# Optimization experiments

Hardware: AMD Instinct MI355X
Metric: run time of the kernel (lower is better)

## Reference

```python
import jax, jax.numpy as jnp
import numpy as np

D_MODEL = 2048
N_HEADS = 16
N_KV = 4
HEAD_DIM = D_MODEL // N_HEADS  # 128
KV_DIM = N_KV * HEAD_DIM       # 512
CLIP = 8.0
EPS = 1e-5
THETA = 500000.0


def setup_inputs() -> dict:
    key = jax.random.key(0)
    ks = jax.random.split(key, 12)
    B, T = 2, 2048
    std = 0.02
    return {
        "x": jax.random.normal(ks[0], (B, T, D_MODEL), jnp.float32),
        "wq": jax.random.normal(ks[1], (D_MODEL, D_MODEL), jnp.float32) * std,
        "bq": jnp.zeros((D_MODEL,), jnp.float32),
        "wk": jax.random.normal(ks[2], (KV_DIM, D_MODEL), jnp.float32) * std,
        "bk": jnp.zeros((KV_DIM,), jnp.float32),
        "wv": jax.random.normal(ks[3], (KV_DIM, D_MODEL), jnp.float32) * std,
        "bv": jnp.zeros((KV_DIM,), jnp.float32),
        "wo": jax.random.normal(ks[4], (D_MODEL, D_MODEL), jnp.float32) * std,
        "bo": jnp.zeros((D_MODEL,), jnp.float32),
        "q_gamma": jnp.ones((D_MODEL,), jnp.float32),
        "q_beta": jnp.zeros((D_MODEL,), jnp.float32),
        "k_gamma": jnp.ones((KV_DIM,), jnp.float32),
        "k_beta": jnp.zeros((KV_DIM,), jnp.float32),
    }


def _layernorm(x, gamma, beta):
    mu = jnp.mean(x, axis=-1, keepdims=True)
    var = jnp.mean(jnp.square(x - mu), axis=-1, keepdims=True)
    return (x - mu) * jax.lax.rsqrt(var + EPS) * gamma + beta


def _rope(q, k):
    # q: (B,T,H,Dh), k: (B,T,Hkv,Dh); non-interleaved rotate-half RoPE
    T = q.shape[1]
    half = HEAD_DIM // 2
    inv_freq = 1.0 / (THETA ** (jnp.arange(0, half, dtype=jnp.float32) * 2.0 / HEAD_DIM))
    freqs = jnp.arange(T, dtype=jnp.float32)[:, None] * inv_freq[None, :]  # (T, half)
    emb = jnp.concatenate([freqs, freqs], axis=-1)  # (T, Dh)
    cos = jnp.cos(emb)[None, :, None, :]
    sin = jnp.sin(emb)[None, :, None, :]

    def rot_half(x):
        x1, x2 = x[..., :half], x[..., half:]
        return jnp.concatenate([-x2, x1], axis=-1)

    q = q * cos + rot_half(q) * sin
    k = k * cos + rot_half(k) * sin
    return q, k


def reference(x, wq, bq, wk, bk, wv, bv, wo, bo, q_gamma, q_beta, k_gamma, k_beta):
    B, T, _ = x.shape
    q = x @ wq.T + bq            # (B,T,D)
    k = x @ wk.T + bk            # (B,T,KV_DIM)
    v = x @ wv.T + bv
    q = jnp.clip(q, -CLIP, CLIP)
    k = jnp.clip(k, -CLIP, CLIP)
    v = jnp.clip(v, -CLIP, CLIP)
    q = _layernorm(q, q_gamma, q_beta)
    k = _layernorm(k, k_gamma, k_beta)
    q = q.reshape(B, T, N_HEADS, HEAD_DIM)
    k = k.reshape(B, T, N_KV, HEAD_DIM)
    v = v.reshape(B, T, N_KV, HEAD_DIM)
    q, k = _rope(q, k)
    # to (B,H,T,Dh)
    q = q.transpose(0, 2, 1, 3)
    k = k.transpose(0, 2, 1, 3)
    v = v.transpose(0, 2, 1, 3)
    g = N_HEADS // N_KV
    # GQA repeat_interleave via broadcast: (B,Hkv,T,Dh) -> (B,H,T,Dh)
    k = jnp.broadcast_to(k[:, :, None], (B, N_KV, g, T, HEAD_DIM)).reshape(B, N_HEADS, T, HEAD_DIM)
    v = jnp.broadcast_to(v[:, :, None], (B, N_KV, g, T, HEAD_DIM)).reshape(B, N_HEADS, T, HEAD_DIM)
    scale = 1.0 / jnp.sqrt(jnp.float32(HEAD_DIM))
    scores = jnp.einsum('bhqd,bhkd->bhqk', q, k) * scale
    causal = jnp.tril(jnp.ones((T, T), dtype=bool))
    scores = jnp.where(causal[None, None], scores, jnp.finfo(scores.dtype).min)
    att = jax.nn.softmax(scores, axis=-1)
    out = jnp.einsum('bhqk,bhkd->bhqd', att, v)     # (B,H,T,Dh)
    out = out.transpose(0, 2, 1, 3).reshape(B, T, D_MODEL)
    return out @ wo.T + bo
```

## Files before the change

### kernel.cpp

```cpp
#include <hip/hip_runtime.h>
#include <hip/hip_bf16.h>
#include <math.h>

typedef __bf16 bf16;
typedef __attribute__((ext_vector_type(8))) bf16 bf16x8;
typedef __attribute__((ext_vector_type(2))) bf16 bf16x2;
typedef __attribute__((ext_vector_type(4))) float f32x4;

#define LOG2E 1.4426950408889634f
#define LOG2_THETA 18.931568569324174f

#if __has_builtin(__builtin_amdgcn_exp2f)
#define EXP2F __builtin_amdgcn_exp2f
#else
#define EXP2F exp2f
#endif

__device__ inline void async_cp16(const void* gptr, void* lptr) {
  __builtin_amdgcn_global_load_lds(
      (const __attribute__((address_space(1))) unsigned int*)gptr,
      (__attribute__((address_space(3))) unsigned int*)lptr, 16, 0, 0);
}

__global__ __launch_bounds__(256) void cast_f32_bf16(
    const float* __restrict__ in, bf16* __restrict__ out, int n) {
  const int i = (blockIdx.x * 256 + threadIdx.x) * 8;
  if (i >= n) return;
  float4 a = *(const float4*)(in + i);
  float4 b = *(const float4*)(in + i + 4);
  bf16x8 o;
  o[0] = (bf16)a.x; o[1] = (bf16)a.y; o[2] = (bf16)a.z; o[3] = (bf16)a.w;
  o[4] = (bf16)b.x; o[5] = (bf16)b.y; o[6] = (bf16)b.z; o[7] = (bf16)b.w;
  *(bf16x8*)(out + i) = o;
}

__global__ __launch_bounds__(256) void gemm_qkv(
    const bf16* __restrict__ A, const bf16* __restrict__ W,
    const float* __restrict__ bq, const float* __restrict__ bk,
    const float* __restrict__ bv, bf16* __restrict__ C,
    int M, int N, int K) {
  __shared__ bf16 As[128 * 32];
  __shared__ bf16 Bs[128 * 32];
  const int m0 = blockIdx.x * 128, n0 = blockIdx.y * 128;
  const int t = threadIdx.x;
  const int w = t >> 6, lane = t & 63, quad = lane >> 4, l15 = lane & 15;
  const int wm = (w >> 1) * 64, wn = (w & 1) * 64;

  f32x4 acc[4][4];
#pragma unroll
  for (int i = 0; i < 4; i++)
#pragma unroll
    for (int j = 0; j < 4; j++) acc[i][j] = (f32x4)0.0f;

  const int rS = t >> 2;
  const int cS = (t & 3) * 8;

  for (int k0 = 0; k0 < K; k0 += 32) {
    async_cp16(A + (size_t)(m0 + rS) * K + k0 + cS, (char*)As + (size_t)(w * 64) * 16);
    async_cp16(A + (size_t)(m0 + 64 + rS) * K + k0 + cS, (char*)As + (size_t)(256 + w * 64) * 16);
    async_cp16(W + (size_t)(n0 + rS) * K + k0 + cS, (char*)Bs + (size_t)(w * 64) * 16);
    async_cp16(W + (size_t)(n0 + 64 + rS) * K + k0 + cS, (char*)Bs + (size_t)(256 + w * 64) * 16);
    __syncthreads();

    bf16x8 af[4], bfr[4];
#pragma unroll
    for (int i = 0; i < 4; i++)
      af[i] = *(const bf16x8*)(As + (wm + i * 16 + l15) * 32 + quad * 8);
#pragma unroll
    for (int j = 0; j < 4; j++)
      bfr[j] = *(const bf16x8*)(Bs + (wn + j * 16 + l15) * 32 + quad * 8);
#pragma unroll
    for (int i = 0; i < 4; i++)
#pragma unroll
      for (int j = 0; j < 4; j++)
        acc[i][j] = __builtin_amdgcn_mfma_f32_16x16x32_bf16(af[i], bfr[j], acc[i][j], 0, 0, 0);
    __syncthreads();
  }

#pragma unroll
  for (int i = 0; i < 4; i++)
#pragma unroll
    for (int j = 0; j < 4; j++) {
      const int col = n0 + wn + j * 16 + l15;
      float bval;
      if (col < 2048) bval = bq[col];
      else if (col < 2560) bval = bk[col - 2048];
      else bval = bv[col - 2560];
#pragma unroll
      for (int r = 0; r < 4; r++) {
        const int row = m0 + wm + i * 16 + quad * 4 + r;
        float v = acc[i][j][r] + bval;
        v = fminf(fmaxf(v, -8.0f), 8.0f);
        C[(size_t)row * N + col] = (bf16)v;
      }
    }
}

template <typename OUT_T, bool CLIP>
__global__ __launch_bounds__(256) void gemm_bt(
    const bf16* __restrict__ A, const bf16* __restrict__ W,
    const float* __restrict__ bias, OUT_T* __restrict__ C,
    int M, int N, int K) {
  __shared__ bf16 As[128 * 32];
  __shared__ bf16 Bs[128 * 32];
  const int m0 = blockIdx.x * 128, n0 = blockIdx.y * 128;
  const int t = threadIdx.x;
  const int w = t >> 6, lane = t & 63, quad = lane >> 4, l15 = lane & 15;
  const int wm = (w >> 1) * 64, wn = (w & 1) * 64;

  f32x4 acc[4][4];
#pragma unroll
  for (int i = 0; i < 4; i++)
#pragma unroll
    for (int j = 0; j < 4; j++) acc[i][j] = (f32x4)0.0f;

  const int rS = t >> 2;
  const int cS = (t & 3) * 8;

  for (int k0 = 0; k0 < K; k0 += 32) {
    async_cp16(A + (size_t)(m0 + rS) * K + k0 + cS, (char*)As + (size_t)(w * 64) * 16);
    async_cp16(A + (size_t)(m0 + 64 + rS) * K + k0 + cS, (char*)As + (size_t)(256 + w * 64) * 16);
    async_cp16(W + (size_t)(n0 + rS) * K + k0 + cS, (char*)Bs + (size_t)(w * 64) * 16);
    async_cp16(W + (size_t)(n0 + 64 + rS) * K + k0 + cS, (char*)Bs + (size_t)(256 + w * 64) * 16);
    __syncthreads();

    bf16x8 af[4], bfr[4];
#pragma unroll
    for (int i = 0; i < 4; i++)
      af[i] = *(const bf16x8*)(As + (wm + i * 16 + l15) * 32 + quad * 8);
#pragma unroll
    for (int j = 0; j < 4; j++)
      bfr[j] = *(const bf16x8*)(Bs + (wn + j * 16 + l15) * 32 + quad * 8);
#pragma unroll
    for (int i = 0; i < 4; i++)
#pragma unroll
      for (int j = 0; j < 4; j++)
        acc[i][j] = __builtin_amdgcn_mfma_f32_16x16x32_bf16(af[i], bfr[j], acc[i][j], 0, 0, 0);
    __syncthreads();
  }

#pragma unroll
  for (int i = 0; i < 4; i++)
#pragma unroll
    for (int j = 0; j < 4; j++) {
      const int col = n0 + wn + j * 16 + l15;
      const float bval = bias[col];
#pragma unroll
      for (int r = 0; r < 4; r++) {
        const int row = m0 + wm + i * 16 + quad * 4 + r;
        float v = acc[i][j][r] + bval;
        if (CLIP) v = fminf(fmaxf(v, -8.0f), 8.0f);
        C[(size_t)row * N + col] = (OUT_T)v;
      }
    }
}

__global__ __launch_bounds__(256) void ln_rope_q(
    const bf16* __restrict__ X, const float* __restrict__ gamma,
    const float* __restrict__ beta, bf16* __restrict__ Q) {
  const int row = blockIdx.x;
  const int b = row >> 11, tpos = row & 2047;
  const bf16* x = X + (size_t)row * 3072;
  __shared__ float sh[2048];
  __shared__ float red[8];
  const int tid = threadIdx.x;
  const int w = tid >> 6, lane = tid & 63;

  bf16x8 xi = *(const bf16x8*)(x + tid * 8);
  float v[8];
  float s = 0.0f;
#pragma unroll
  for (int e = 0; e < 8; e++) { v[e] = (float)xi[e]; s += v[e]; }
#pragma unroll
  for (int m = 32; m >= 1; m >>= 1) s += __shfl_xor(s, m, 64);
  if (lane == 0) red[w] = s;
  __syncthreads();
  const float mean = (red[0] + red[1] + red[2] + red[3]) * (1.0f / 2048.0f);
  float vs = 0.0f;
#pragma unroll
  for (int e = 0; e < 8; e++) { float d = v[e] - mean; vs += d * d; }
#pragma unroll
  for (int m = 32; m >= 1; m >>= 1) vs += __shfl_xor(vs, m, 64);
  if (lane == 0) red[4 + w] = vs;
  __syncthreads();
  const float var = (red[4] + red[5] + red[6] + red[7]) * (1.0f / 2048.0f);
  const float rstd = rsqrtf(var + 1e-5f);
#pragma unroll
  for (int e = 0; e < 8; e++) {
    const int c = tid * 8 + e;
    const float y = (v[e] - mean) * rstd * gamma[c] + beta[c];
    sh[c] = y; v[e] = y;
  }
  __syncthreads();

  const int c0 = tid * 8;
  const int h = c0 >> 7;
  bf16x8 ov;
#pragma unroll
  for (int e = 0; e < 8; e++) {
    const int c = c0 + e, d = c & 127, i = d & 63;
    const float inv = exp2f((float)i * (-LOG2_THETA / 64.0f));
    float sn, cs;
    sincosf((float)tpos * inv, &sn, &cs);
    const float rot = (d < 64) ? -sh[c + 64] : sh[c - 64];
    ov[e] = (bf16)(v[e] * cs + rot * sn);
  }
  *(bf16x8*)(Q + ((size_t)(b * 16 + h) * 2048 + tpos) * 128 + (c0 & 127)) = ov;
}

__global__ __launch_bounds__(256) void ln_rope_k(
    const bf16* __restrict__ X, const float* __restrict__ gamma,
    const float* __restrict__ beta, bf16* __restrict__ Ko) {
  const int row = blockIdx.x;
  const int b = row >> 11, tpos = row & 2047;
  const bf16* x = X + (size_t)row * 3072 + 2048;
  __shared__ float sh[512];
  __shared__ float red[8];
  const int tid = threadIdx.x;
  const int w = tid >> 6, lane = tid & 63;

  bf16x2 xi = *(const bf16x2*)(x + tid * 2);
  float v0 = (float)xi[0], v1 = (float)xi[1];
  float s = v0 + v1;
#pragma unroll
  for (int m = 32; m >= 1; m >>= 1) s += __shfl_xor(s, m, 64);
  if (lane == 0) red[w] = s;
  __syncthreads();
  const float mean = (red[0] + red[1] + red[2] + red[3]) * (1.0f / 512.0f);
  float d0 = v0 - mean, d1 = v1 - mean;
  float vs = d0 * d0 + d1 * d1;
#pragma unroll
  for (int m = 32; m >= 1; m >>= 1) vs += __shfl_xor(vs, m, 64);
  if (lane == 0) red[4 + w] = vs;
  __syncthreads();
  const float var = (red[4] + red[5] + red[6] + red[7]) * (1.0f / 512.0f);
  const float rstd = rsqrtf(var + 1e-5f);
  const int c0 = tid * 2;
  float y0 = d0 * rstd * gamma[c0] + beta[c0];
  float y1 = d1 * rstd * gamma[c0 + 1] + beta[c0 + 1];
  sh[c0] = y0; sh[c0 + 1] = y1;
  __syncthreads();

  const int kv = c0 >> 7;
  float yy[2] = {y0, y1};
  bf16x2 ov;
#pragma unroll
  for (int e = 0; e < 2; e++) {
    const int c = c0 + e, d = c & 127, i = d & 63;
    const float inv = exp2f((float)i * (-LOG2_THETA / 64.0f));
    float sn, cs;
    sincosf((float)tpos * inv, &sn, &cs);
    const float rot = (d < 64) ? -sh[c + 64] : sh[c - 64];
    ov[e] = (bf16)(yy[e] * cs + rot * sn);
  }
  *(bf16x2*)(Ko + ((size_t)(b * 4 + kv) * 2048 + tpos) * 128 + (c0 & 127)) = ov;
}

__global__ __launch_bounds__(256) void transpose_v(
    const bf16* __restrict__ V, bf16* __restrict__ Vt) {
  const int t0 = blockIdx.x * 64, kv = blockIdx.y, b = blockIdx.z;
  __shared__ bf16 tile[64][136];
  const int tid = threadIdx.x;
#pragma unroll
  for (int i = 0; i < 4; i++) {
    const int c = i * 256 + tid;
    const int r = c >> 4, d8 = (c & 15) * 8;
    *(bf16x8*)&tile[r][d8] =
        *(const bf16x8*)(V + (size_t)(b * 2048 + t0 + r) * 3072 + 2560 + kv * 128 + d8);
  }
  __syncthreads();
#pragma unroll
  for (int i = 0; i < 4; i++) {
    const int c = i * 256 + tid;
    const int d = c >> 3, t8 = (c & 7) * 8;
    bf16x8 o;
#pragma unroll
    for (int j = 0; j < 8; j++) o[j] = tile[t8 + j][d];
    *(bf16x8*)(Vt + (size_t)((b * 4 + kv) * 128 + d) * 2048 + t0 + t8) = o;
  }
}

__global__ __launch_bounds__(256) void flash_attn(
    const bf16* __restrict__ Q, const bf16* __restrict__ Kt,
    const bf16* __restrict__ Vt, bf16* __restrict__ O) {
  const int p = blockIdx.x;
  const int h = blockIdx.y, b = blockIdx.z;
  const int kv = h >> 2;
  const int tid = threadIdx.x;
  const int w = tid >> 6, lane = tid & 63, quad = lane >> 4, l15 = lane & 15;

  __shared__ bf16 Ks[64][128];
  __shared__ bf16 Vs[128][64];
  __shared__ bf16 Ps[4][16][88];

  const bf16* Kb = Kt + (size_t)(b * 4 + kv) * 2048 * 128;
  const bf16* Vb = Vt + (size_t)(b * 4 + kv) * 128 * 2048;

  const int ksl = lane & 15, krt = lane >> 4;
  const int vsl = lane & 7,  vdt = lane >> 3;
  int okff[4], ovff[4];
#pragma unroll
  for (int i = 0; i < 4; i++) {
    const int c = w * 4 + i;
    const int rt = c * 4 + krt;
    okff[i] = rt * 128 + ((ksl ^ (rt & 15)) * 8);
    const int d = c * 8 + vdt;
    ovff[i] = d * 2048 + ((vsl ^ (d & 7)) * 8);
  }

  const float cexp = 0.08838834764831845f * LOG2E;
  bf16x8 ones;
#pragma unroll
  for (int i = 0; i < 8; i++) ones[i] = (bf16)1.0f;

#pragma unroll 1
  for (int pass = 0; pass < 2; pass++) {
    const int qb = (pass == 0) ? (31 - p) : p;
    const int q0 = qb * 64;
    const int nkt = qb + 1;

    const bf16* Qb = Q + ((size_t)(b * 16 + h) * 2048 + q0 + w * 16 + l15) * 128;
    bf16x8 aq[4];
#pragma unroll
    for (int kk = 0; kk < 4; kk++) aq[kk] = *(const bf16x8*)(Qb + kk * 32 + quad * 8);

    f32x4 o[9];
#pragma unroll
    for (int dt = 0; dt < 9; dt++) o[dt] = (f32x4)0.0f;

#pragma unroll 1
    for (int kt = 0; kt < nkt; kt++) {
      const int k0 = kt * 64;
      __syncthreads();
      {
        const size_t kbase = (size_t)k0 * 128;
#pragma unroll
        for (int i = 0; i < 4; i++) {
          const int c = w * 4 + i;
          async_cp16(Kb + kbase + okff[i], (char*)&Ks[0][0] + c * 1024);
          async_cp16(Vb + (size_t)k0 + ovff[i], (char*)&Vs[0][0] + c * 1024);
        }
      }
      __syncthreads();

      f32x4 s4[4];
#pragma unroll
      for (int j = 0; j < 4; j++) {
        f32x4 acc = (f32x4)0.0f;
        const int n = j * 16 + l15;
#pragma unroll
        for (int kk = 0; kk < 4; kk++) {
          bf16x8 bk = *(const bf16x8*)(
              &Ks[0][0] + n * 128 + (((kk * 4 + quad) ^ l15) * 8));
          acc = __builtin_amdgcn_mfma_f32_16x16x32_bf16(aq[kk], bk, acc, 0, 0, 0);
        }
        s4[j] = acc;
      }

      const bool diag = (kt == qb);
      const int qrow_base = q0 + w * 16 + quad * 4;
#pragma unroll
      for (int j = 0; j < 4; j++) {
        const int kg = k0 + j * 16 + l15;
#pragma unroll
        for (int r = 0; r < 4; r++) {
          float pv = EXP2F(s4[j][r] * cexp);
          if (diag && kg > qrow_base + r) pv = 0.0f;
          Ps[w][quad * 4 + r][j * 16 + l15] = (bf16)pv;
        }
      }
      __asm__ volatile("s_waitcnt lgkmcnt(0)" ::: "memory");

#pragma unroll
      for (int kk = 0; kk < 2; kk++) {
        bf16x8 pa = *(const bf16x8*)&Ps[w][l15][kk * 32 + quad * 8];
#pragma unroll
        for (int dt = 0; dt < 8; dt++) {
          const int d = dt * 16 + l15;
          bf16x8 vb = *(const bf16x8*)(
              &Vs[0][0] + d * 64 + (((kk * 4 + quad) ^ (d & 7)) * 8));
          o[dt] = __builtin_amdgcn_mfma_f32_16x16x32_bf16(pa, vb, o[dt], 0, 0, 0);
        }
        o[8] = __builtin_amdgcn_mfma_f32_16x16x32_bf16(pa, ones, o[8], 0, 0, 0);
      }
    }

    bf16* Ob = O + ((size_t)(b * 2048 + q0 + w * 16 + quad * 4)) * 2048 + h * 128;
#pragma unroll
    for (int r = 0; r < 4; r++) {
      const float rinv = 1.0f / o[8][r];
#pragma unroll
      for (int dt = 0; dt < 8; dt++)
        Ob[(size_t)r * 2048 + dt * 16 + l15] = (bf16)(o[dt][r] * rinv);
    }
  }
}

extern "C" void kernel_launch(void* const* d_in, const int* in_sizes, int n_in,
                              void* d_out, int out_size, void* d_ws, size_t ws_size,
                              hipStream_t stream) {
  const float* x   = (const float*)d_in[0];
  const float* wq  = (const float*)d_in[1];
  const float* bq  = (const float*)d_in[2];
  const float* wk  = (const float*)d_in[3];
  const float* bk  = (const float*)d_in[4];
  const float* wv  = (const float*)d_in[5];
  const float* bv  = (const float*)d_in[6];
  const float* wo  = (const float*)d_in[7];
  const float* bo  = (const float*)d_in[8];
  const float* qg  = (const float*)d_in[9];
  const float* qbt = (const float*)d_in[10];
  const float* kg  = (const float*)d_in[11];
  const float* kbt = (const float*)d_in[12];
  float* out = (float*)d_out;

  char* ws = (char*)d_ws;
  if (ws_size < (size_t)88080384) return;
  bf16* xb    = (bf16*)(ws);
  bf16* wqkvb = (bf16*)(ws + 16777216);
  bf16* wob   = (bf16*)(ws + 29360128);
  bf16* qkvb  = (bf16*)(ws + 37748736);
  bf16* Qr    = (bf16*)(ws + 62914560);
  bf16* Kr    = (bf16*)(ws + 79691776);
  bf16* Vt    = (bf16*)(ws + 83886080);
  bf16* At    = (bf16*)(ws);

  cast_f32_bf16<<<4096, 256, 0, stream>>>(x,  xb, 8388608);
  cast_f32_bf16<<<2048, 256, 0, stream>>>(wq, wqkvb, 4194304);
  cast_f32_bf16<<<512,  256, 0, stream>>>(wk, wqkvb + (size_t)2048 * 2048, 1048576);
  cast_f32_bf16<<<512,  256, 0, stream>>>(wv, wqkvb + (size_t)2560 * 2048, 1048576);
  cast_f32_bf16<<<2048, 256, 0, stream>>>(wo, wob, 4194304);

  gemm_qkv<<<dim3(32, 24), 256, 0, stream>>>(xb, wqkvb, bq, bk, bv, qkvb, 4096, 3072, 2048);
  ln_rope_q<<<4096, 256, 0, stream>>>(qkvb, qg, qbt, Qr);
  ln_rope_k<<<4096, 256, 0, stream>>>(qkvb, kg, kbt, Kr);
  transpose_v<<<dim3(32, 4, 2), 256, 0, stream>>>(qkvb, Vt);
  flash_attn<<<dim3(16, 16, 2), 256, 0, stream>>>(Qr, Kr, Vt, At);
  gemm_bt<float, false><<<dim3(32, 16), 256, 0, stream>>>(At, wob, bo, out, 4096, 2048, 2048);
}
```

Before: 352.5 us.

## Merge cast and mid-stage kernels, widen GEMM K tile with swizzled LDS

Result: faster. 329.8 us (-6.4%).

```diff
diff --git a/kernel.cpp b/kernel.cpp
--- a/kernel.cpp
+++ b/kernel.cpp
@@ -22,28 +22,40 @@
       (__attribute__((address_space(3))) unsigned int*)lptr, 16, 0, 0);
 }
 
-__global__ __launch_bounds__(256) void cast_f32_bf16(
-    const float* __restrict__ in, bf16* __restrict__ out, int n) {
-  const int i = (blockIdx.x * 256 + threadIdx.x) * 8;
-  if (i >= n) return;
-  float4 a = *(const float4*)(in + i);
-  float4 b = *(const float4*)(in + i + 4);
+__global__ __launch_bounds__(256) void cast_all(
+    const float* __restrict__ x,  const float* __restrict__ wq,
+    const float* __restrict__ wk, const float* __restrict__ wv,
+    const float* __restrict__ wo, bf16* __restrict__ xb,
+    bf16* __restrict__ wqkvb, bf16* __restrict__ wob) {
+  const int bx = blockIdx.x;
+  const size_t gi = ((size_t)bx * 256 + threadIdx.x) * 8;
+  const float* src;
+  bf16* dst;
+  if (bx < 4096)      { src = x  + gi;              dst = xb + gi; }
+  else if (bx < 6144) { src = wq + (gi -  8388608); dst = wqkvb + (gi - 8388608); }
+  else if (bx < 6656) { src = wk + (gi - 12582912); dst = wqkvb + 4194304 + (gi - 12582912); }
+  else if (bx < 7168) { src = wv + (gi - 13631488); dst = wqkvb + 5242880 + (gi - 13631488); }
+  else                { src = wo + (gi - 14680064); dst = wob + (gi - 14680064); }
+  float4 a = *(const float4*)(src);
+  float4 b = *(const float4*)(src + 4);
   bf16x8 o;
   o[0] = (bf16)a.x; o[1] = (bf16)a.y; o[2] = (bf16)a.z; o[3] = (bf16)a.w;
   o[4] = (bf16)b.x; o[5] = (bf16)b.y; o[6] = (bf16)b.z; o[7] = (bf16)b.w;
-  *(bf16x8*)(out + i) = o;
-}
-
-__global__ __launch_bounds__(256) void gemm_qkv(
+  *(bf16x8*)dst = o;
+}
+
+template <typename OUT_T, bool QKV, bool CLIP>
+__global__ __launch_bounds__(256) void gemm_bt(
     const bf16* __restrict__ A, const bf16* __restrict__ W,
-    const float* __restrict__ bq, const float* __restrict__ bk,
-    const float* __restrict__ bv, bf16* __restrict__ C,
+    const float* __restrict__ b0, const float* __restrict__ b1,
+    const float* __restrict__ b2, OUT_T* __restrict__ C,
     int M, int N, int K) {
-  __shared__ bf16 As[128 * 32];
-  __shared__ bf16 Bs[128 * 32];
+  __shared__ bf16 As[128 * 64];
+  __shared__ bf16 Bs[128 * 64];
   const int m0 = blockIdx.x * 128, n0 = blockIdx.y * 128;
   const int t = threadIdx.x;
   const int w = t >> 6, lane = t & 63, quad = lane >> 4, l15 = lane & 15;
+  const int sw = l15 & 7;
   const int wm = (w >> 1) * 64, wn = (w & 1) * 64;
 
   f32x4 acc[4][4];
@@ -52,28 +64,43 @@
 #pragma unroll
     for (int j = 0; j < 4; j++) acc[i][j] = (f32x4)0.0f;
 
-  const int rS = t >> 2;
-  const int cS = (t & 3) * 8;
-
-  for (int k0 = 0; k0 < K; k0 += 32) {
-    async_cp16(A + (size_t)(m0 + rS) * K + k0 + cS, (char*)As + (size_t)(w * 64) * 16);
-    async_cp16(A + (size_t)(m0 + 64 + rS) * K + k0 + cS, (char*)As + (size_t)(256 + w * 64) * 16);
-    async_cp16(W + (size_t)(n0 + rS) * K + k0 + cS, (char*)Bs + (size_t)(w * 64) * 16);
-    async_cp16(W + (size_t)(n0 + 64 + rS) * K + k0 + cS, (char*)Bs + (size_t)(256 + w * 64) * 16);
-    __syncthreads();
-
-    bf16x8 af[4], bfr[4];
-#pragma unroll
-    for (int i = 0; i < 4; i++)
-      af[i] = *(const bf16x8*)(As + (wm + i * 16 + l15) * 32 + quad * 8);
-#pragma unroll
-    for (int j = 0; j < 4; j++)
-      bfr[j] = *(const bf16x8*)(Bs + (wn + j * 16 + l15) * 32 + quad * 8);
-#pragma unroll
-    for (int i = 0; i < 4; i++)
+  int soff[4];
+#pragma unroll
+  for (int i = 0; i < 4; i++) {
+    const int c = w * 256 + i * 64 + lane;
+    const int r = c >> 3;
+    const int sl = (c & 7) ^ (r & 7);
+    soff[i] = r * K + sl * 8;
+  }
+  const bf16* Abase = A + (size_t)m0 * K;
+  const bf16* Wbase = W + (size_t)n0 * K;
+
+  for (int k0 = 0; k0 < K; k0 += 64) {
+#pragma unroll
+    for (int i = 0; i < 4; i++) {
+      const int dst = (w * 256 + i * 64) * 16;
+      async_cp16(Abase + k0 + soff[i], (char*)As + dst);
+      async_cp16(Wbase + k0 + soff[i], (char*)Bs + dst);
+    }
+    __syncthreads();
+
+#pragma unroll
+    for (int kk = 0; kk < 2; kk++) {
+      bf16x8 af[4], bfr[4];
+#pragma unroll
+      for (int i = 0; i < 4; i++)
+        af[i] = *(const bf16x8*)(As + (wm + i * 16 + l15) * 64 +
+                                 (((kk * 4 + quad) ^ sw) * 8));
 #pragma unroll
       for (int j = 0; j < 4; j++)
-        acc[i][j] = __builtin_amdgcn_mfma_f32_16x16x32_bf16(af[i], bfr[j], acc[i][j], 0, 0, 0);
+        bfr[j] = *(const bf16x8*)(Bs + (wn + j * 16 + l15) * 64 +
+                                  (((kk * 4 + quad) ^ sw) * 8));
+#pragma unroll
+      for (int i = 0; i < 4; i++)
+#pragma unroll
+        for (int j = 0; j < 4; j++)
+          acc[i][j] = __builtin_amdgcn_mfma_f32_16x16x32_bf16(af[i], bfr[j], acc[i][j], 0, 0, 0);
+    }
     __syncthreads();
   }
 
@@ -83,68 +110,13 @@
     for (int j = 0; j < 4; j++) {
       const int col = n0 + wn + j * 16 + l15;
       float bval;
-      if (col < 2048) bval = bq[col];
-      else if (col < 2560) bval = bk[col - 2048];
-      else bval = bv[col - 2560];
-#pragma unroll
-      for (int r = 0; r < 4; r++) {
-        const int row = m0 + wm + i * 16 + quad * 4 + r;
-        float v = acc[i][j][r] + bval;
-        v = fminf(fmaxf(v, -8.0f), 8.0f);
-        C[(size_t)row * N + col] = (bf16)v;
-      }
-    }
-}
-
-template <typename OUT_T, bool CLIP>
-__global__ __launch_bounds__(256) void gemm_bt(
-    const bf16* __restrict__ A, const bf16* __restrict__ W,
-    const float* __restrict__ bias, OUT_T* __restrict__ C,
-    int M, int N, int K) {
-  __shared__ bf16 As[128 * 32];
-  __shared__ bf16 Bs[128 * 32];
-  const int m0 = blockIdx.x * 128, n0 = blockIdx.y * 128;
-  const int t = threadIdx.x;
-  const int w = t >> 6, lane = t & 63, quad = lane >> 4, l15 = lane & 15;
-  const int wm = (w >> 1) * 64, wn = (w & 1) * 64;
-
-  f32x4 acc[4][4];
-#pragma unroll
-  for (int i = 0; i < 4; i++)
-#pragma unroll
-    for (int j = 0; j < 4; j++) acc[i][j] = (f32x4)0.0f;
-
-  const int rS = t >> 2;
-  const int cS = (t & 3) * 8;
-
-  for (int k0 = 0; k0 < K; k0 += 32) {
-    async_cp16(A + (size_t)(m0 + rS) * K + k0 + cS, (char*)As + (size_t)(w * 64) * 16);
-    async_cp16(A + (size_t)(m0 + 64 + rS) * K + k0 + cS, (char*)As + (size_t)(256 + w * 64) * 16);
-    async_cp16(W + (size_t)(n0 + rS) * K + k0 + cS, (char*)Bs + (size_t)(w * 64) * 16);
-    async_cp16(W + (size_t)(n0 + 64 + rS) * K + k0 + cS, (char*)Bs + (size_t)(256 + w * 64) * 16);
-    __syncthreads();
-
-    bf16x8 af[4], bfr[4];
-#pragma unroll
-    for (int i = 0; i < 4; i++)
-      af[i] = *(const bf16x8*)(As + (wm + i * 16 + l15) * 32 + quad * 8);
-#pragma unroll
-    for (int j = 0; j < 4; j++)
-      bfr[j] = *(const bf16x8*)(Bs + (wn + j * 16 + l15) * 32 + quad * 8);
-#pragma unroll
-    for (int i = 0; i < 4; i++)
-#pragma unroll
-      for (int j = 0; j < 4; j++)
-        acc[i][j] = __builtin_amdgcn_mfma_f32_16x16x32_bf16(af[i], bfr[j], acc[i][j], 0, 0, 0);
-    __syncthreads();
-  }
-
-#pragma unroll
-  for (int i = 0; i < 4; i++)
-#pragma unroll
-    for (int j = 0; j < 4; j++) {
-      const int col = n0 + wn + j * 16 + l15;
-      const float bval = bias[col];
+      if (QKV) {
+        if (col < 2048) bval = b0[col];
+        else if (col < 2560) bval = b1[col - 2048];
+        else bval = b2[col - 2560];
+      } else {
+        bval = b0[col];
+      }
 #pragma unroll
       for (int r = 0; r < 4; r++) {
         const int row = m0 + wm + i * 16 + quad * 4 + r;
@@ -155,128 +127,117 @@
     }
 }
 
-__global__ __launch_bounds__(256) void ln_rope_q(
-    const bf16* __restrict__ X, const float* __restrict__ gamma,
-    const float* __restrict__ beta, bf16* __restrict__ Q) {
-  const int row = blockIdx.x;
-  const int b = row >> 11, tpos = row & 2047;
-  const bf16* x = X + (size_t)row * 3072;
-  __shared__ float sh[2048];
-  __shared__ float red[8];
+__global__ __launch_bounds__(256) void fused_mid(
+    const bf16* __restrict__ X, const float* __restrict__ qg,
+    const float* __restrict__ qb, const float* __restrict__ kg,
+    const float* __restrict__ kb, bf16* __restrict__ Qr,
+    bf16* __restrict__ Kr, bf16* __restrict__ Vt) {
+  __shared__ float smf[2056];
+  __shared__ bf16 smt[64][136];
+  const int bx = blockIdx.x;
   const int tid = threadIdx.x;
   const int w = tid >> 6, lane = tid & 63;
-
-  bf16x8 xi = *(const bf16x8*)(x + tid * 8);
-  float v[8];
-  float s = 0.0f;
-#pragma unroll
-  for (int e = 0; e < 8; e++) { v[e] = (float)xi[e]; s += v[e]; }
-#pragma unroll
-  for (int m = 32; m >= 1; m >>= 1) s += __shfl_xor(s, m, 64);
-  if (lane == 0) red[w] = s;
-  __syncthreads();
-  const float mean = (red[0] + red[1] + red[2] + red[3]) * (1.0f / 2048.0f);
-  float vs = 0.0f;
-#pragma unroll
-  for (int e = 0; e < 8; e++) { float d = v[e] - mean; vs += d * d; }
-#pragma unroll
-  for (int m = 32; m >= 1; m >>= 1) vs += __shfl_xor(vs, m, 64);
-  if (lane == 0) red[4 + w] = vs;
-  __syncthreads();
-  const float var = (red[4] + red[5] + red[6] + red[7]) * (1.0f / 2048.0f);
-  const float rstd = rsqrtf(var + 1e-5f);
-#pragma unroll
-  for (int e = 0; e < 8; e++) {
-    const int c = tid * 8 + e;
-    const float y = (v[e] - mean) * rstd * gamma[c] + beta[c];
-    sh[c] = y; v[e] = y;
-  }
-  __syncthreads();
-
-  const int c0 = tid * 8;
-  const int h = c0 >> 7;
-  bf16x8 ov;
-#pragma unroll
-  for (int e = 0; e < 8; e++) {
-    const int c = c0 + e, d = c & 127, i = d & 63;
-    const float inv = exp2f((float)i * (-LOG2_THETA / 64.0f));
-    float sn, cs;
-    sincosf((float)tpos * inv, &sn, &cs);
-    const float rot = (d < 64) ? -sh[c + 64] : sh[c - 64];
-    ov[e] = (bf16)(v[e] * cs + rot * sn);
-  }
-  *(bf16x8*)(Q + ((size_t)(b * 16 + h) * 2048 + tpos) * 128 + (c0 & 127)) = ov;
-}
-
-__global__ __launch_bounds__(256) void ln_rope_k(
-    const bf16* __restrict__ X, const float* __restrict__ gamma,
-    const float* __restrict__ beta, bf16* __restrict__ Ko) {
-  const int row = blockIdx.x;
-  const int b = row >> 11, tpos = row & 2047;
-  const bf16* x = X + (size_t)row * 3072 + 2048;
-  __shared__ float sh[512];
-  __shared__ float red[8];
-  const int tid = threadIdx.x;
-  const int w = tid >> 6, lane = tid & 63;
-
-  bf16x2 xi = *(const bf16x2*)(x + tid * 2);
-  float v0 = (float)xi[0], v1 = (float)xi[1];
-  float s = v0 + v1;
-#pragma unroll
-  for (int m = 32; m >= 1; m >>= 1) s += __shfl_xor(s, m, 64);
-  if (lane == 0) red[w] = s;
-  __syncthreads();
-  const float mean = (red[0] + red[1] + red[2] + red[3]) * (1.0f / 512.0f);
-  float d0 = v0 - mean, d1 = v1 - mean;
-  float vs = d0 * d0 + d1 * d1;
-#pragma unroll
-  for (int m = 32; m >= 1; m >>= 1) vs += __shfl_xor(vs, m, 64);
-  if (lane == 0) red[4 + w] = vs;
-  __syncthreads();
-  const float var = (red[4] + red[5] + red[6] + red[7]) * (1.0f / 512.0f);
-  const float rstd = rsqrtf(var + 1e-5f);
-  const int c0 = tid * 2;
-  float y0 = d0 * rstd * gamma[c0] + beta[c0];
-  float y1 = d1 * rstd * gamma[c0 + 1] + beta[c0 + 1];
-  sh[c0] = y0; sh[c0 + 1] = y1;
-  __syncthreads();
-
-  const int kv = c0 >> 7;
-  float yy[2] = {y0, y1};
-  bf16x2 ov;
-#pragma unroll
-  for (int e = 0; e < 2; e++) {
-    const int c = c0 + e, d = c & 127, i = d & 63;
-    const float inv = exp2f((float)i * (-LOG2_THETA / 64.0f));
-    float sn, cs;
-    sincosf((float)tpos * inv, &sn, &cs);
-    const float rot = (d < 64) ? -sh[c + 64] : sh[c - 64];
-    ov[e] = (bf16)(yy[e] * cs + rot * sn);
-  }
-  *(bf16x2*)(Ko + ((size_t)(b * 4 + kv) * 2048 + tpos) * 128 + (c0 & 127)) = ov;
-}
-
-__global__ __launch_bounds__(256) void transpose_v(
-    const bf16* __restrict__ V, bf16* __restrict__ Vt) {
-  const int t0 = blockIdx.x * 64, kv = blockIdx.y, b = blockIdx.z;
-  __shared__ bf16 tile[64][136];
-  const int tid = threadIdx.x;
-#pragma unroll
-  for (int i = 0; i < 4; i++) {
-    const int c = i * 256 + tid;
-    const int r = c >> 4, d8 = (c & 15) * 8;
-    *(bf16x8*)&tile[r][d8] =
-        *(const bf16x8*)(V + (size_t)(b * 2048 + t0 + r) * 3072 + 2560 + kv * 128 + d8);
-  }
-  __syncthreads();
-#pragma unroll
-  for (int i = 0; i < 4; i++) {
-    const int c = i * 256 + tid;
-    const int d = c >> 3, t8 = (c & 7) * 8;
-    bf16x8 o;
-#pragma unroll
-    for (int j = 0; j < 8; j++) o[j] = tile[t8 + j][d];
-    *(bf16x8*)(Vt + (size_t)((b * 4 + kv) * 128 + d) * 2048 + t0 + t8) = o;
+  float* red = smf + 2048;
+
+  if (bx < 4096) {
+    const int row = bx, b = row >> 11, tpos = row & 2047;
+    const bf16* x = X + (size_t)row * 3072;
+    bf16x8 xi = *(const bf16x8*)(x + tid * 8);
+    float v[8];
+    float s = 0.0f;
+#pragma unroll
+    for (int e = 0; e < 8; e++) { v[e] = (float)xi[e]; s += v[e]; }
+#pragma unroll
+    for (int m = 32; m >= 1; m >>= 1) s += __shfl_xor(s, m, 64);
+    if (lane == 0) red[w] = s;
+    __syncthreads();
+    const float mean = (red[0] + red[1] + red[2] + red[3]) * (1.0f / 2048.0f);
+    float vs = 0.0f;
+#pragma unroll
+    for (int e = 0; e < 8; e++) { float d = v[e] - mean; vs += d * d; }
+#pragma unroll
+    for (int m = 32; m >= 1; m >>= 1) vs += __shfl_xor(vs, m, 64);
+    if (lane == 0) red[4 + w] = vs;
+    __syncthreads();
+    const float var = (red[4] + red[5] + red[6] + red[7]) * (1.0f / 2048.0f);
+    const float rstd = rsqrtf(var + 1e-5f);
+#pragma unroll
+    for (int e = 0; e < 8; e++) {
+      const int c = tid * 8 + e;
+      const float y = (v[e] - mean) * rstd * qg[c] + qb[c];
+      smf[c] = y; v[e] = y;
+    }
+    __syncthreads();
+    const int c0 = tid * 8;
+    const int h = c0 >> 7;
+    bf16x8 ov;
+#pragma unroll
+    for (int e = 0; e < 8; e++) {
+      const int c = c0 + e, d = c & 127, i = d & 63;
+      const float inv = exp2f((float)i * (-LOG2_THETA / 64.0f));
+      float sn, cs;
+      sincosf((float)tpos * inv, &sn, &cs);
+      const float rot = (d < 64) ? -smf[c + 64] : smf[c - 64];
+      ov[e] = (bf16)(v[e] * cs + rot * sn);
+    }
+    *(bf16x8*)(Qr + ((size_t)(b * 16 + h) * 2048 + tpos) * 128 + (c0 & 127)) = ov;
+  } else if (bx < 8192) {
+    const int row = bx - 4096, b = row >> 11, tpos = row & 2047;
+    const bf16* x = X + (size_t)row * 3072 + 2048;
+    bf16x2 xi = *(const bf16x2*)(x + tid * 2);
+    float v0 = (float)xi[0], v1 = (float)xi[1];
+    float s = v0 + v1;
+#pragma unroll
+    for (int m = 32; m >= 1; m >>= 1) s += __shfl_xor(s, m, 64);
+    if (lane == 0) red[w] = s;
+    __syncthreads();
+    const float mean = (red[0] + red[1] + red[2] + red[3]) * (1.0f / 512.0f);
+    float d0 = v0 - mean, d1 = v1 - mean;
+    float vs = d0 * d0 + d1 * d1;
+#pragma unroll
+    for (int m = 32; m >= 1; m >>= 1) vs += __shfl_xor(vs, m, 64);
+    if (lane == 0) red[4 + w] = vs;
+    __syncthreads();
+    const float var = (red[4] + red[5] + red[6] + red[7]) * (1.0f / 512.0f);
+    const float rstd = rsqrtf(var + 1e-5f);
+    const int c0 = tid * 2;
+    float y0 = d0 * rstd * kg[c0] + kb[c0];
+    float y1 = d1 * rstd * kg[c0 + 1] + kb[c0 + 1];
+    smf[c0] = y0; smf[c0 + 1] = y1;
+    __syncthreads();
+    const int kv = c0 >> 7;
+    float yy[2] = {y0, y1};
+    bf16x2 ov;
+#pragma unroll
+    for (int e = 0; e < 2; e++) {
+      const int c = c0 + e, d = c & 127, i = d & 63;
+      const float inv = exp2f((float)i * (-LOG2_THETA / 64.0f));
+      float sn, cs;
+      sincosf((float)tpos * inv, &sn, &cs);
+      const float rot = (d < 64) ? -smf[c + 64] : smf[c - 64];
+      ov[e] = (bf16)(yy[e] * cs + rot * sn);
+    }
+    *(bf16x2*)(Kr + ((size_t)(b * 4 + kv) * 2048 + tpos) * 128 + (c0 & 127)) = ov;
+  } else {
+    const int idx = bx - 8192;
+    const int b = idx >> 7, kv = (idx >> 5) & 3, t0 = (idx & 31) * 64;
+#pragma unroll
+    for (int i = 0; i < 4; i++) {
+      const int c = i * 256 + tid;
+      const int r = c >> 4, d8 = (c & 15) * 8;
+      *(bf16x8*)&smt[r][d8] =
+          *(const bf16x8*)(X + (size_t)(b * 2048 + t0 + r) * 3072 + 2560 + kv * 128 + d8);
+    }
+    __syncthreads();
+#pragma unroll
+    for (int i = 0; i < 4; i++) {
+      const int c = i * 256 + tid;
+      const int d = c >> 3, t8 = (c & 7) * 8;
+      bf16x8 o;
+#pragma unroll
+      for (int j = 0; j < 8; j++) o[j] = smt[t8 + j][d];
+      *(bf16x8*)(Vt + (size_t)((b * 4 + kv) * 128 + d) * 2048 + t0 + t8) = o;
+    }
   }
 }
 
@@ -425,16 +386,11 @@
   bf16* Vt    = (bf16*)(ws + 83886080);
   bf16* At    = (bf16*)(ws);
 
-  cast_f32_bf16<<<4096, 256, 0, stream>>>(x,  xb, 8388608);
-  cast_f32_bf16<<<2048, 256, 0, stream>>>(wq, wqkvb, 4194304);
-  cast_f32_bf16<<<512,  256, 0, stream>>>(wk, wqkvb + (size_t)2048 * 2048, 1048576);
-  cast_f32_bf16<<<512,  256, 0, stream>>>(wv, wqkvb + (size_t)2560 * 2048, 1048576);
-  cast_f32_bf16<<<2048, 256, 0, stream>>>(wo, wob, 4194304);
-
-  gemm_qkv<<<dim3(32, 24), 256, 0, stream>>>(xb, wqkvb, bq, bk, bv, qkvb, 4096, 3072, 2048);
-  ln_rope_q<<<4096, 256, 0, stream>>>(qkvb, qg, qbt, Qr);
-  ln_rope_k<<<4096, 256, 0, stream>>>(qkvb, kg, kbt, Kr);
-  transpose_v<<<dim3(32, 4, 2), 256, 0, stream>>>(qkvb, Vt);
+  cast_all<<<9216, 256, 0, stream>>>(x, wq, wk, wv, wo, xb, wqkvb, wob);
+  gemm_bt<bf16, true, true><<<dim3(32, 24), 256, 0, stream>>>(
+      xb, wqkvb, bq, bk, bv, qkvb, 4096, 3072, 2048);
+  fused_mid<<<8448, 256, 0, stream>>>(qkvb, qg, qbt, kg, kbt, Qr, Kr, Vt);
   flash_attn<<<dim3(16, 16, 2), 256, 0, stream>>>(Qr, Kr, Vt, At);
-  gemm_bt<float, false><<<dim3(32, 16), 256, 0, stream>>>(At, wob, bo, out, 4096, 2048, 2048);
-}
+  gemm_bt<float, false, false><<<dim3(32, 16), 256, 0, stream>>>(
+      At, wob, bo, nullptr, nullptr, out, 4096, 2048, 2048);
+}
```
